# Optimization experiments

Measured on AMD Instinct MI355X. Metric: run time of the kernel, lower is better.

Reference implementation:

```python
import jax, jax.numpy as jnp
import numpy as np

C = 1.0          # curvature of PoincareBall
SQRT_C = 1.0
MIN_NORM = 1e-15
PROJ_EPS = 4e-3  # float32 boundary eps used by PoincareBall.proj
N_NODES = 50000


def _norm(x):
    return jnp.clip(jnp.linalg.norm(x, axis=-1, keepdims=True), MIN_NORM)


def _artanh(x):
    return jnp.arctanh(jnp.clip(x, -1.0 + 1e-7, 1.0 - 1e-7))


def proj(x):
    # clip points to the open ball of radius (1-eps)/sqrt(c)
    norm = _norm(x)
    maxnorm = (1.0 - PROJ_EPS) / SQRT_C
    return jnp.where(norm > maxnorm, x / norm * maxnorm, x)


def expmap0(u):
    u_norm = _norm(u)
    return jnp.tanh(SQRT_C * u_norm) * u / (SQRT_C * u_norm)


def logmap0(p):
    p_norm = _norm(p)
    return _artanh(SQRT_C * p_norm) * p / (SQRT_C * p_norm)


def mobius_add(x, y):
    x2 = jnp.sum(x * x, -1, keepdims=True)
    y2 = jnp.sum(y * y, -1, keepdims=True)
    xy = jnp.sum(x * y, -1, keepdims=True)
    num = (1.0 + 2.0 * C * xy + C * y2) * x + (1.0 - C * x2) * y
    den = 1.0 + 2.0 * C * xy + C * C * x2 * y2
    return num / jnp.clip(den, MIN_NORM)


def mobius_matvec(m, x):
    x_norm = _norm(x)
    mx = x @ m.T  # [N, d_out]
    mx_norm = _norm(mx)
    res = jnp.tanh(mx_norm / x_norm * _artanh(SQRT_C * x_norm)) * mx / (mx_norm * SQRT_C)
    zero_row = jnp.all(mx == 0, axis=-1, keepdims=True)
    return jnp.where(zero_row, jnp.zeros_like(res), res)


def setup_inputs() -> dict:
    key = jax.random.key(0)
    k = jax.random.split(key, 6)
    n, d_in, d_out, n_edges = N_NODES, 256, 96, 800000
    # points on the Poincare ball
    x = proj(0.02 * jax.random.normal(k[0], (n, d_in), jnp.float32))
    weight = jax.random.normal(k[1], (d_out, d_in), jnp.float32) * (1.0 / np.sqrt(d_in)).astype(np.float32)
    bias = jax.random.normal(k[2], (d_out,), jnp.float32) * 0.01
    edge_row = jax.random.randint(k[3], (n_edges,), 0, n)
    edge_col = jax.random.randint(k[4], (n_edges,), 0, n)
    # normalized adjacency weights ~ 1/avg_degree
    edge_weight = jax.random.uniform(k[5], (n_edges,), jnp.float32) * (1.0 / 16.0)
    return {"x": x, "weight": weight, "bias": bias, "edge_weight": edge_weight,
            "edge_row": edge_row, "edge_col": edge_col}


def reference(x, weight, bias, edge_weight, edge_row, edge_col):
    # --- HypLinear (dropout inactive in eval) ---
    h = proj(mobius_matvec(weight, x))
    hyp_bias = proj(expmap0(bias[None, :]))  # proj_tan0 is identity on the ball
    h = proj(mobius_add(h, hyp_bias))
    # --- HypAgg: spmm(adj, logmap0(h)) then expmap0 ---
    xt = logmap0(h)                                  # [N, d_out]
    msgs = edge_weight[:, None] * xt[edge_col]       # [E, d_out]
    support = jax.ops.segment_sum(msgs, edge_row, num_segments=N_NODES)
    h = proj(expmap0(support))
    # --- HypAct: relu in tangent space, map back (c_in == c_out) ---
    h = proj(expmap0(jax.nn.relu(logmap0(h))))
    return h
```

## Files before the change

kernel.cpp:

```cpp
#include <hip/hip_runtime.h>


typedef __attribute__((ext_vector_type(8))) short short8;
typedef __attribute__((ext_vector_type(4))) float floatx4;

#define DIN 256
#define DOUT 96
#define MAXN 0.996f
#define EPS15 1e-15f
#define ATC (1.0f - 1e-7f)
#define NBK 391
#define CAP 3072
#define TILE 3072

__device__ __forceinline__ float us2f(unsigned short u) {
    unsigned int v = ((unsigned int)u) << 16;
    return __uint_as_float(v);
}
__device__ __forceinline__ unsigned short f2us(float f) {
    unsigned int b = __float_as_uint(f);
    unsigned int r = (b + 0x7FFFu + ((b >> 16) & 1u)) >> 16;
    return (unsigned short)r;
}

__global__ void initzero_kernel(const unsigned short* __restrict__ xraw,
                                const void* __restrict__ bias,
                                const void* __restrict__ wgt,
                                float* __restrict__ ws,
                                int* __restrict__ gcur) {
    int i = blockIdx.x * blockDim.x + threadIdx.x;
    int stride = gridDim.x * blockDim.x;
    for (int k = i; k < NBK * 16; k += stride) gcur[k] = 0;

    if (blockIdx.x == 0 && threadIdx.x < 64) {
        int l = threadIdx.x;
        float v0 = us2f(xraw[l]);
        float v1 = us2f(xraw[64 + l]);
        int big = (!(fabsf(v0) < 1e4f)) || (!(fabsf(v1) < 1e4f));
        #pragma unroll
        for (int m = 32; m >= 1; m >>= 1) big |= __shfl_xor(big, m, 64);
        bool isb = !big;
        if (l == 0) ws[97] = isb ? 1.0f : 0.0f;

        float b0 = isb ? us2f(((const unsigned short*)bias)[l])
                       : ((const float*)bias)[l];
        float b1 = 0.0f;
        if (l < 32)
            b1 = isb ? us2f(((const unsigned short*)bias)[64 + l])
                     : ((const float*)bias)[64 + l];
        float n2 = b0 * b0 + b1 * b1;
        #pragma unroll
        for (int m = 32; m >= 1; m >>= 1) n2 += __shfl_xor(n2, m, 64);
        float bn = fmaxf(sqrtf(n2), EPS15);
        float ef = tanhf(bn) / bn;
        float hn = ef * sqrtf(n2);
        float s = (hn > MAXN) ? MAXN / fmaxf(hn, EPS15) : 1.0f;
        ws[l] = s * ef * b0;
        if (l < 32) ws[64 + l] = s * ef * b1;
        if (l == 0) { float v = s * hn; ws[96] = v * v; }
    }

    if (blockIdx.x >= 1 && blockIdx.x <= 12) {
        int t = threadIdx.x, lane = t & 63;
        float v0 = us2f(xraw[lane]);
        float v1 = us2f(xraw[64 + lane]);
        int big = (!(fabsf(v0) < 1e4f)) || (!(fabsf(v1) < 1e4f));
        #pragma unroll
        for (int m = 32; m >= 1; m >>= 1) big |= __shfl_xor(big, m, 64);
        bool isb = !big;
        uint4* wz = (uint4*)(ws + 128);
        int g = t + 256 * (int)(blockIdx.x - 1);
        int c = g >> 5, j = g & 31;
        int f = c >> 4, mr = c & 15;
        int kt = j >> 2, q = j & 3;
        if (isb) {
            const uint4* wg = (const uint4*)wgt;
            wz[(f * 8 + kt) * 64 + q * 16 + mr] = wg[g];
        } else {
            const float* wgf = (const float*)wgt;
            const float* src = wgf + (size_t)c * DIN + j * 8;
            unsigned short tmp[8];
            #pragma unroll
            for (int z = 0; z < 8; z++) tmp[z] = f2us(src[z]);
            wz[(f * 8 + kt) * 64 + q * 16 + mr] = *(const uint4*)tmp;
        }
    }
}

__global__ void __launch_bounds__(256) part_kernel(
        const void* __restrict__ ew,
        const int* __restrict__ erow,
        const int* __restrict__ ecol,
        const float* __restrict__ ws,
        int* __restrict__ gcur,
        uint2* __restrict__ arena, int E) {
    __shared__ uint2 stage[TILE];
    __shared__ int h[NBK], excl[NBK], cur[NBK], gb[NBK];
    __shared__ int cb[64];

    const int t = threadIdx.x;
    const bool isb = ws[97] != 0.0f;
    const int tb = blockIdx.x * TILE;
    const int tcnt = min(TILE, E - tb);

    for (int i = t; i < NBK; i += 256) h[i] = 0;
    __syncthreads();

    int rw[12]; unsigned int pk[12];
    #pragma unroll
    for (int k = 0; k < 12; k++) {
        int e = tb + t + 256 * k;
        if (e < E) {
            int r = erow[e];
            unsigned int wb = isb ? (unsigned int)((const unsigned short*)ew)[e]
                                  : (unsigned int)f2us(((const float*)ew)[e]);
            rw[k] = r;
            pk[k] = (wb << 16) | (unsigned int)ecol[e];
            atomicAdd(&h[r >> 7], 1);
        } else rw[k] = -1;
    }
    __syncthreads();

    if (t < 64) {
        int s = 0;
        #pragma unroll
        for (int j = 0; j < 8; j++) {
            int b2 = t * 8 + j;
            if (b2 < NBK) s += h[b2];
        }
        int sc = s;
        #pragma unroll
        for (int d = 1; d < 64; d <<= 1) {
            int tt = __shfl_up(sc, d, 64);
            if (t >= d) sc += tt;
        }
        cb[t] = sc - s;
    }
    __syncthreads();
    for (int b2 = t; b2 < NBK; b2 += 256) {
        int base = cb[b2 >> 3];
        int x = 0;
        for (int j = (b2 & ~7); j < b2; j++) x += h[j];
        excl[b2] = base + x;
        cur[b2]  = base + x;
        gb[b2] = atomicAdd(&gcur[b2 * 16], h[b2]);
    }
    __syncthreads();

    #pragma unroll
    for (int k = 0; k < 12; k++) {
        if (rw[k] >= 0) {
            int b2 = rw[k] >> 7;
            int slot = atomicAdd(&cur[b2], 1);
            stage[slot] = make_uint2(pk[k], (unsigned int)rw[k]);
        }
    }
    __syncthreads();

    for (int s = t; s < tcnt; s += 256) {
        uint2 ent = stage[s];
        int b2 = (int)ent.y >> 7;
        int p = gb[b2] + (s - excl[b2]);
        if (p < CAP) arena[(size_t)b2 * CAP + p] = ent;
    }
}

__global__ void hyp_kernel(const void* __restrict__ x,
                           float* __restrict__ ws,
                           unsigned short* __restrict__ xtb,
                           int N) {
    const int t = threadIdx.x;
    const bool isb = ws[97] != 0.0f;
    const int lane = t & 63;
    const int wv = t >> 6;
    const int mrow = lane & 15;
    const int quad = lane >> 4;
    const uint4* __restrict__ Wg = (const uint4*)(ws + 128);

    const int r0 = ((int)blockIdx.x * 4 + wv) * 16;
    if (r0 >= N) return;

    float hbl[6];
    #pragma unroll
    for (int f = 0; f < 6; f++) hbl[f] = ws[mrow + 16 * f];
    const float hb2 = ws[96];

    int xr = r0 + mrow; if (xr >= N) xr = N - 1;
    short8 afrag[8];
    if (isb) {
        const unsigned short* xrow = (const unsigned short*)x + (size_t)xr * DIN + quad * 8;
        #pragma unroll
        for (int kt = 0; kt < 8; kt++)
            afrag[kt] = *(const short8*)(xrow + kt * 32);
    } else {
        const float* xrow = (const float*)x + (size_t)xr * DIN + quad * 8;
        #pragma unroll
        for (int kt = 0; kt < 8; kt++) {
            short8 a;
            #pragma unroll
            for (int j = 0; j < 8; j++) a[j] = (short)f2us(xrow[kt * 32 + j]);
            afrag[kt] = a;
        }
    }

    float xn2p = 0.f;
    #pragma unroll
    for (int kt = 0; kt < 8; kt++)
        #pragma unroll
        for (int j = 0; j < 8; j++) {
            float v = us2f((unsigned short)afrag[kt][j]);
            xn2p = fmaf(v, v, xn2p);
        }
    xn2p += __shfl_xor(xn2p, 16, 64);
    xn2p += __shfl_xor(xn2p, 32, 64);

    floatx4 acc[6];
    #pragma unroll
    for (int f = 0; f < 6; f++) acc[f] = (floatx4){0.f, 0.f, 0.f, 0.f};
    #pragma unroll
    for (int f = 0; f < 6; f++) {
        uint4 bw[8];
        #pragma unroll
        for (int kt = 0; kt < 8; kt++)
            bw[kt] = Wg[(f * 8 + kt) * 64 + lane];
        #pragma unroll
        for (int kt = 0; kt < 8; kt++) {
            short8 bfr = *(const short8*)&bw[kt];
            acc[f] = __builtin_amdgcn_mfma_f32_16x16x32_bf16(afrag[kt], bfr, acc[f], 0, 0, 0);
        }
    }

    float mxn2[4], dmh[4];
    #pragma unroll
    for (int reg = 0; reg < 4; reg++) {
        float a2 = 0.f, ad = 0.f;
        #pragma unroll
        for (int f = 0; f < 6; f++) {
            float v = acc[f][reg];
            a2 = fmaf(v, v, a2);
            ad = fmaf(v, hbl[f], ad);
        }
        mxn2[reg] = a2; dmh[reg] = ad;
    }
    #pragma unroll
    for (int m = 8; m >= 1; m >>= 1)
        #pragma unroll
        for (int reg = 0; reg < 4; reg++) {
            mxn2[reg] += __shfl_xor(mxn2[reg], m, 64);
            dmh[reg]  += __shfl_xor(dmh[reg],  m, 64);
        }

    int sel = mrow & 3;
    float xn2  = __shfl(xn2p, quad * 4 + sel, 64);
    float wmx2 = mxn2[sel], wdmh = dmh[sel];

    float xn  = fmaxf(sqrtf(xn2), EPS15);
    float mxn = fmaxf(sqrtf(wmx2), EPS15);
    float g   = (mxn / xn) * atanhf(fminf(xn, ATC));
    float tg  = tanhf(g);
    float rs0 = tg / mxn;
    float rn  = rs0 * sqrtf(wmx2);
    float s1  = (rn > MAXN) ? MAXN / fmaxf(rn, EPS15) : 1.0f;
    float al  = s1 * rs0;
    float x2  = al * al * wmx2;
    float xy  = al * wdmh;
    float cA  = 1.0f + 2.0f * xy + hb2;
    float cB  = 1.0f - x2;
    float den = fmaxf(1.0f + 2.0f * xy + x2 * hb2, EPS15);
    float p   = cA * al / den;
    float qq  = cB / den;
    float o2  = p*p*wmx2 + 2.0f*p*qq*wdmh + qq*qq*hb2;
    float on  = sqrtf(fmaxf(o2, 0.0f));
    float s2  = (on > MAXN) ? MAXN / fmaxf(on, EPS15) : 1.0f;
    float pn  = fmaxf(s2 * on, EPS15);
    float F   = (atanhf(fminf(pn, ATC)) / pn) * s2;
    float Fp_m = F * p, Fq_m = F * qq;

    float Fp[4], Fq[4];
    #pragma unroll
    for (int reg = 0; reg < 4; reg++) {
        Fp[reg] = __shfl(Fp_m, quad * 16 + reg, 64);
        Fq[reg] = __shfl(Fq_m, quad * 16 + reg, 64);
    }

    #pragma unroll
    for (int reg = 0; reg < 4; reg++) {
        int row = r0 + quad * 4 + reg;
        if (row < N) {
            size_t base = (size_t)row * DOUT + mrow;
            #pragma unroll
            for (int f = 0; f < 6; f++)
                xtb[base + 16 * f] = f2us(fmaf(Fp[reg], acc[f][reg], Fq[reg] * hbl[f]));
        }
    }
}

__global__ void __launch_bounds__(256) sortg_kernel(
        const int* __restrict__ gcur,
        uint2* __restrict__ arena,
        uint2* __restrict__ roff) {
    __shared__ int h[128], h8[128], excl[128], cur[128];

    const int t = threadIdx.x;
    const int idx = blockIdx.x;
    int cnt = gcur[idx * 16]; if (cnt > CAP) cnt = CAP;
    const size_t ab = (size_t)idx * CAP;

    for (int i = t; i < 128; i += 256) h[i] = 0;
    __syncthreads();

    uint2 ent[12];
    #pragma unroll
    for (int k = 0; k < 12; k++) {
        int j = t + 256 * k;
        if (j < cnt) {
            ent[k] = arena[ab + j];
            atomicAdd(&h[ent[k].y & 127u], 1);
        } else ent[k] = make_uint2(0u, 0u);
    }
    __syncthreads();

    if (t < 64) {
        int a0 = h[2 * t], a1 = h[2 * t + 1];
        int p0 = (a0 + 7) & ~7, p1 = (a1 + 7) & ~7;
        int ps = p0 + p1;
        int sc = ps;
        #pragma unroll
        for (int d = 1; d < 64; d <<= 1) {
            int tt = __shfl_up(sc, d, 64);
            if (t >= d) sc += tt;
        }
        int ex = sc - ps;
        h8[2 * t] = p0;        h8[2 * t + 1] = p1;
        excl[2 * t] = ex;      excl[2 * t + 1] = ex + p0;
        cur[2 * t]  = ex;      cur[2 * t + 1]  = ex + p0;
    }
    __syncthreads();

    if (t < 128) {
        int e8 = excl[t];
        int c8 = h8[t];
        if (e8 > CAP) e8 = CAP;
        if (e8 + c8 > CAP) c8 = CAP - e8;
        if (c8 < 0) c8 = 0;
        roff[idx * 128 + t] =
            make_uint2((unsigned int)(ab + e8), (unsigned int)c8);
        for (int j = excl[t] + h[t]; j < excl[t] + h8[t]; j++)
            if (j < CAP) arena[ab + j] = make_uint2(0u, 0u);
    }
    #pragma unroll
    for (int k = 0; k < 12; k++) {
        int j = t + 256 * k;
        if (j < cnt) {
            int slot = atomicAdd(&cur[ent[k].y & 127u], 1);
            if (slot < CAP)
                arena[ab + slot] =
                    make_uint2((ent[k].x & 0xFFFFu) * 192u,
                               ent[k].x & 0xFFFF0000u);
        }
    }
}

__global__ void __launch_bounds__(256) rowagg_kernel(
        const unsigned short* __restrict__ xtb,
        const uint2* __restrict__ arena,
        const uint2* __restrict__ roff,
        const float* __restrict__ ws,
        void* __restrict__ out, int N) {
    int wv = threadIdx.x >> 6, lane = threadIdx.x & 63;
    int node = blockIdx.x * 4 + wv;
    if (node >= N) return;
    const bool isb = ws[97] != 0.0f;
    const bool act = lane < 48;

    uint2 ro = roff[node];
    unsigned int start = ro.x;
    int cnt8 = (int)ro.y;

    const char* __restrict__ xc = (const char*)xtb;
    const unsigned int lane4 = (unsigned int)lane * 4u;

    float acc0 = 0.f, acc1 = 0.f;
    unsigned int uA[8], uB[8];
    float wA[8], wB[8];

#define ISSUE(BU, BW, B)                                                       \
    _Pragma("unroll")                                                          \
    for (int k = 0; k < 8; k++) {                                              \
        int idx = (B) * 8 + k;                                                 \
        unsigned int off = (unsigned int)__shfl((int)my.x, idx, 64);           \
        BW[k] = __uint_as_float((unsigned int)__shfl((int)my.y, idx, 64));     \
        BU[k] = *(const unsigned int*)(xc + off + lane4);                      \
    }

#define CONSUME(BU, BW)                                                        \
    _Pragma("unroll")                                                          \
    for (int k = 0; k < 8; k++) {                                              \
        acc0 = fmaf(BW[k], __uint_as_float(BU[k] << 16), acc0);                \
        acc1 = fmaf(BW[k], __uint_as_float(BU[k] & 0xFFFF0000u), acc1);        \
    }

    for (int cs = 0; cs < cnt8; cs += 64) {
        int navail = cnt8 - cs; if (navail > 64) navail = 64;
        uint2 my = arena[start + cs + lane];
        int nb = navail >> 3;
        ISSUE(uA, wA, 0);
        for (int bb = 1; bb < nb; bb++) {
            if (bb & 1) { ISSUE(uB, wB, bb); CONSUME(uA, wA); }
            else        { ISSUE(uA, wA, bb); CONSUME(uB, wB); }
        }
        if (nb & 1) { CONSUME(uA, wA); }
        else        { CONSUME(uB, wB); }
    }
#undef ISSUE
#undef CONSUME

    if (!act) { acc0 = 0.f; acc1 = 0.f; }

    float u0 = acc0, u1 = acc1;
    float n2 = u0*u0 + u1*u1;
    #pragma unroll
    for (int m = 32; m >= 1; m >>= 1) n2 += __shfl_xor(n2, m, 64);
    float un = fmaxf(sqrtf(n2), EPS15);
    float ef = tanhf(un) / un;
    float p0 = ef * u0, p1 = ef * u1;
    float pnrm = ef * sqrtf(n2);
    float sc = (pnrm > MAXN) ? MAXN / fmaxf(pnrm, EPS15) : 1.0f;
    p0 *= sc; p1 *= sc; pnrm *= sc;
    float pncl = fmaxf(pnrm, EPS15);
    float lf = atanhf(fminf(pncl, ATC)) / pncl;
    float t0 = fmaxf(lf * p0, 0.0f), t1 = fmaxf(lf * p1, 0.0f);
    float tn2 = t0*t0 + t1*t1;
    #pragma unroll
    for (int m = 32; m >= 1; m >>= 1) tn2 += __shfl_xor(tn2, m, 64);
    float tn = fmaxf(sqrtf(tn2), EPS15);
    float ef2 = tanhf(tn) / tn;
    float en = ef2 * sqrtf(tn2);
    float s2 = (en > MAXN) ? MAXN / fmaxf(en, EPS15) : 1.0f;
    float scale = s2 * ef2;
    float v0 = scale * t0, v1 = scale * t1;

    if (act) {
        if (isb) {
            unsigned int pk = ((unsigned int)f2us(v1) << 16) | (unsigned int)f2us(v0);
            ((unsigned int*)((unsigned short*)out + (size_t)node * DOUT))[lane] = pk;
        } else {
            float2 fv; fv.x = v0; fv.y = v1;
            ((float2*)((float*)out + (size_t)node * DOUT))[lane] = fv;
        }
    }
}

extern "C" void kernel_launch(void* const* d_in, const int* in_sizes, int n_in,
                              void* d_out, int out_size, void* d_ws, size_t ws_size,
                              hipStream_t stream) {
    const void* x    = d_in[0];
    const void* wgt  = d_in[1];
    const void* bias = d_in[2];
    const void* ew   = d_in[3];
    const int* erow  = (const int*)d_in[4];
    const int* ecol  = (const int*)d_in[5];

    int N = out_size / DOUT;
    int E = in_sizes[4];

    float* wsf = (float*)d_ws;
    int* gcur = (int*)(wsf + 128 + 12288);
    uint2* arena = (uint2*)((char*)d_ws + 74688);
    unsigned short* xtb = (unsigned short*)((char*)d_ws + 74688 + (size_t)NBK * CAP * 8);
    uint2* roff = (uint2*)(xtb + (size_t)N * DOUT);

    int Pb = (E + TILE - 1) / TILE;
    int Hb = (N + 63) / 64;

    initzero_kernel<<<13, 256, 0, stream>>>((const unsigned short*)x, bias, wgt, wsf, gcur);
    part_kernel<<<Pb, 256, 0, stream>>>(ew, erow, ecol, wsf, gcur, arena, E);
    hyp_kernel<<<Hb, 256, 0, stream>>>(x, wsf, xtb, N);
    sortg_kernel<<<NBK, 256, 0, stream>>>(gcur, arena, roff);
    rowagg_kernel<<<(N + 3) / 4, 256, 0, stream>>>(xtb, arena, roff, wsf, d_out, N);
}
```

Before: 184.2 us.

## Fuse pipeline stages into one persistent cooperative kernel with grid syncs

Merges the five separate launches (init, partition, hyperbolic linear, bucket sort, row aggregation) into a single persistent cooperative mega-kernel. Stages are separated by grid-wide barriers, and each stage's work is spread over a grid capped at 1024 blocks, with hyp work and bucket sorting sharing one phase. The partition tile shrinks to fit the shared-memory budget for four blocks per CU. The aim is to remove per-launch overhead and inter-kernel gaps. In exchange it adds grid-sync costs and gives the grid-stride loops less parallelism than the original per-kernel grids, with a multi-launch fallback if cooperative launch fails.

```diff
diff --git a/kernel.cpp b/kernel.cpp
--- a/kernel.cpp
+++ b/kernel.cpp
@@ -1,4 +1,7 @@
 #include <hip/hip_runtime.h>
+#include <hip/hip_cooperative_groups.h>
+
+namespace cg = cooperative_groups;
 
 
 typedef __attribute__((ext_vector_type(8))) short short8;
@@ -11,7 +14,7 @@
 #define ATC (1.0f - 1e-7f)
 #define NBK 391
 #define CAP 3072
-#define TILE 3072
+#define TILE 1024
 
 __device__ __forceinline__ float us2f(unsigned short u) {
     unsigned int v = ((unsigned int)u) << 16;
@@ -23,25 +26,13 @@
     return (unsigned short)r;
 }
 
-__global__ void initzero_kernel(const unsigned short* __restrict__ xraw,
-                                const void* __restrict__ bias,
-                                const void* __restrict__ wgt,
-                                float* __restrict__ ws,
-                                int* __restrict__ gcur) {
-    int i = blockIdx.x * blockDim.x + threadIdx.x;
-    int stride = gridDim.x * blockDim.x;
-    for (int k = i; k < NBK * 16; k += stride) gcur[k] = 0;
-
-    if (blockIdx.x == 0 && threadIdx.x < 64) {
-        int l = threadIdx.x;
-        float v0 = us2f(xraw[l]);
-        float v1 = us2f(xraw[64 + l]);
-        int big = (!(fabsf(v0) < 1e4f)) || (!(fabsf(v1) < 1e4f));
-        #pragma unroll
-        for (int m = 32; m >= 1; m >>= 1) big |= __shfl_xor(big, m, 64);
-        bool isb = !big;
-        if (l == 0) ws[97] = isb ? 1.0f : 0.0f;
-
+__device__ void phase0(const void* bias, const void* wgt,
+                       float* ws, int* gcur, bool isb,
+                       int bid, int t, int G) {
+    for (int k = bid * 256 + t; k < NBK * 16; k += G * 256) gcur[k] = 0;
+
+    if (bid == 0 && t < 64) {
+        int l = t;
         float b0 = isb ? us2f(((const unsigned short*)bias)[l])
                        : ((const float*)bias)[l];
         float b1 = 0.0f;
@@ -59,17 +50,9 @@
         if (l < 32) ws[64 + l] = s * ef * b1;
         if (l == 0) { float v = s * hn; ws[96] = v * v; }
     }
-
-    if (blockIdx.x >= 1 && blockIdx.x <= 12) {
-        int t = threadIdx.x, lane = t & 63;
-        float v0 = us2f(xraw[lane]);
-        float v1 = us2f(xraw[64 + lane]);
-        int big = (!(fabsf(v0) < 1e4f)) || (!(fabsf(v1) < 1e4f));
-        #pragma unroll
-        for (int m = 32; m >= 1; m >>= 1) big |= __shfl_xor(big, m, 64);
-        bool isb = !big;
+    if (bid >= 1 && bid <= 12) {
         uint4* wz = (uint4*)(ws + 128);
-        int g = t + 256 * (int)(blockIdx.x - 1);
+        int g = t + 256 * (bid - 1);
         int c = g >> 5, j = g & 31;
         int f = c >> 4, mr = c & 15;
         int kt = j >> 2, q = j & 3;
@@ -87,302 +70,290 @@
     }
 }
 
-__global__ void __launch_bounds__(256) part_kernel(
-        const void* __restrict__ ew,
-        const int* __restrict__ erow,
-        const int* __restrict__ ecol,
-        const float* __restrict__ ws,
-        int* __restrict__ gcur,
-        uint2* __restrict__ arena, int E) {
-    __shared__ uint2 stage[TILE];
-    __shared__ int h[NBK], excl[NBK], cur[NBK], gb[NBK];
-    __shared__ int cb[64];
-
-    const int t = threadIdx.x;
-    const bool isb = ws[97] != 0.0f;
-    const int tb = blockIdx.x * TILE;
-    const int tcnt = min(TILE, E - tb);
-
-    for (int i = t; i < NBK; i += 256) h[i] = 0;
-    __syncthreads();
-
-    int rw[12]; unsigned int pk[12];
-    #pragma unroll
-    for (int k = 0; k < 12; k++) {
-        int e = tb + t + 256 * k;
-        if (e < E) {
-            int r = erow[e];
-            unsigned int wb = isb ? (unsigned int)((const unsigned short*)ew)[e]
-                                  : (unsigned int)f2us(((const float*)ew)[e]);
-            rw[k] = r;
-            pk[k] = (wb << 16) | (unsigned int)ecol[e];
-            atomicAdd(&h[r >> 7], 1);
-        } else rw[k] = -1;
-    }
-    __syncthreads();
-
-    if (t < 64) {
-        int s = 0;
+__device__ void phase1(const void* ew, const int* erow, const int* ecol,
+                       int* gcur, uint2* arena, int E, bool isb,
+                       int bid, int t, int G,
+                       uint2* stage, int* sh_h, int* sh_e, int* sh_c,
+                       int* sh_g, int* cb) {
+    for (int tile = bid; tile * TILE < E; tile += G) {
+        const int tb = tile * TILE;
+        const int tcnt = min(TILE, E - tb);
+
+        for (int i = t; i < NBK; i += 256) sh_h[i] = 0;
+        __syncthreads();
+
+        int rw[4]; unsigned int pk[4];
         #pragma unroll
-        for (int j = 0; j < 8; j++) {
-            int b2 = t * 8 + j;
-            if (b2 < NBK) s += h[b2];
-        }
-        int sc = s;
+        for (int k = 0; k < 4; k++) {
+            int e = tb + t + 256 * k;
+            if (e < E) {
+                int r = erow[e];
+                unsigned int wb = isb ? (unsigned int)((const unsigned short*)ew)[e]
+                                      : (unsigned int)f2us(((const float*)ew)[e]);
+                rw[k] = r;
+                pk[k] = (wb << 16) | (unsigned int)ecol[e];
+                atomicAdd(&sh_h[r >> 7], 1);
+            } else rw[k] = -1;
+        }
+        __syncthreads();
+
+        if (t < 64) {
+            int s = 0;
+            #pragma unroll
+            for (int j = 0; j < 8; j++) {
+                int b2 = t * 8 + j;
+                if (b2 < NBK) s += sh_h[b2];
+            }
+            int sc = s;
+            #pragma unroll
+            for (int d = 1; d < 64; d <<= 1) {
+                int tt = __shfl_up(sc, d, 64);
+                if (t >= d) sc += tt;
+            }
+            cb[t] = sc - s;
+        }
+        __syncthreads();
+        for (int b2 = t; b2 < NBK; b2 += 256) {
+            int base = cb[b2 >> 3];
+            int xx = 0;
+            for (int j = (b2 & ~7); j < b2; j++) xx += sh_h[j];
+            sh_e[b2] = base + xx;
+            sh_c[b2] = base + xx;
+            sh_g[b2] = atomicAdd(&gcur[b2 * 16], sh_h[b2]);
+        }
+        __syncthreads();
+
         #pragma unroll
-        for (int d = 1; d < 64; d <<= 1) {
-            int tt = __shfl_up(sc, d, 64);
-            if (t >= d) sc += tt;
-        }
-        cb[t] = sc - s;
-    }
-    __syncthreads();
-    for (int b2 = t; b2 < NBK; b2 += 256) {
-        int base = cb[b2 >> 3];
-        int x = 0;
-        for (int j = (b2 & ~7); j < b2; j++) x += h[j];
-        excl[b2] = base + x;
-        cur[b2]  = base + x;
-        gb[b2] = atomicAdd(&gcur[b2 * 16], h[b2]);
-    }
-    __syncthreads();
-
-    #pragma unroll
-    for (int k = 0; k < 12; k++) {
-        if (rw[k] >= 0) {
-            int b2 = rw[k] >> 7;
-            int slot = atomicAdd(&cur[b2], 1);
-            stage[slot] = make_uint2(pk[k], (unsigned int)rw[k]);
-        }
-    }
-    __syncthreads();
-
-    for (int s = t; s < tcnt; s += 256) {
-        uint2 ent = stage[s];
-        int b2 = (int)ent.y >> 7;
-        int p = gb[b2] + (s - excl[b2]);
-        if (p < CAP) arena[(size_t)b2 * CAP + p] = ent;
-    }
-}
-
-__global__ void hyp_kernel(const void* __restrict__ x,
-                           float* __restrict__ ws,
-                           unsigned short* __restrict__ xtb,
-                           int N) {
-    const int t = threadIdx.x;
-    const bool isb = ws[97] != 0.0f;
+        for (int k = 0; k < 4; k++) {
+            if (rw[k] >= 0) {
+                int b2 = rw[k] >> 7;
+                int slot = atomicAdd(&sh_c[b2], 1);
+                stage[slot] = make_uint2(pk[k], (unsigned int)rw[k]);
+            }
+        }
+        __syncthreads();
+
+        for (int s = t; s < tcnt; s += 256) {
+            uint2 ent = stage[s];
+            int b2 = (int)ent.y >> 7;
+            int p = sh_g[b2] + (s - sh_e[b2]);
+            if (p < CAP) arena[(size_t)b2 * CAP + p] = ent;
+        }
+        __syncthreads();
+    }
+}
+
+__device__ void phase2(const void* x, float* ws, unsigned short* xtb,
+                       const int* gcur, uint2* arena, uint2* roff,
+                       int N, bool isb, int bid, int t, int G,
+                       int* sh_h, int* sh_e, int* sh_c, int* sh_g) {
     const int lane = t & 63;
     const int wv = t >> 6;
-    const int mrow = lane & 15;
-    const int quad = lane >> 4;
-    const uint4* __restrict__ Wg = (const uint4*)(ws + 128);
-
-    const int r0 = ((int)blockIdx.x * 4 + wv) * 16;
-    if (r0 >= N) return;
-
-    float hbl[6];
-    #pragma unroll
-    for (int f = 0; f < 6; f++) hbl[f] = ws[mrow + 16 * f];
-    const float hb2 = ws[96];
-
-    int xr = r0 + mrow; if (xr >= N) xr = N - 1;
-    short8 afrag[8];
-    if (isb) {
-        const unsigned short* xrow = (const unsigned short*)x + (size_t)xr * DIN + quad * 8;
-        #pragma unroll
-        for (int kt = 0; kt < 8; kt++)
-            afrag[kt] = *(const short8*)(xrow + kt * 32);
-    } else {
-        const float* xrow = (const float*)x + (size_t)xr * DIN + quad * 8;
-        #pragma unroll
-        for (int kt = 0; kt < 8; kt++) {
-            short8 a;
-            #pragma unroll
-            for (int j = 0; j < 8; j++) a[j] = (short)f2us(xrow[kt * 32 + j]);
-            afrag[kt] = a;
-        }
-    }
-
-    float xn2p = 0.f;
-    #pragma unroll
-    for (int kt = 0; kt < 8; kt++)
-        #pragma unroll
-        for (int j = 0; j < 8; j++) {
-            float v = us2f((unsigned short)afrag[kt][j]);
-            xn2p = fmaf(v, v, xn2p);
-        }
-    xn2p += __shfl_xor(xn2p, 16, 64);
-    xn2p += __shfl_xor(xn2p, 32, 64);
-
-    floatx4 acc[6];
-    #pragma unroll
-    for (int f = 0; f < 6; f++) acc[f] = (floatx4){0.f, 0.f, 0.f, 0.f};
-    #pragma unroll
-    for (int f = 0; f < 6; f++) {
-        uint4 bw[8];
-        #pragma unroll
-        for (int kt = 0; kt < 8; kt++)
-            bw[kt] = Wg[(f * 8 + kt) * 64 + lane];
-        #pragma unroll
-        for (int kt = 0; kt < 8; kt++) {
-            short8 bfr = *(const short8*)&bw[kt];
-            acc[f] = __builtin_amdgcn_mfma_f32_16x16x32_bf16(afrag[kt], bfr, acc[f], 0, 0, 0);
-        }
-    }
-
-    float mxn2[4], dmh[4];
-    #pragma unroll
-    for (int reg = 0; reg < 4; reg++) {
-        float a2 = 0.f, ad = 0.f;
-        #pragma unroll
-        for (int f = 0; f < 6; f++) {
-            float v = acc[f][reg];
-            a2 = fmaf(v, v, a2);
-            ad = fmaf(v, hbl[f], ad);
-        }
-        mxn2[reg] = a2; dmh[reg] = ad;
-    }
-    #pragma unroll
-    for (int m = 8; m >= 1; m >>= 1)
-        #pragma unroll
-        for (int reg = 0; reg < 4; reg++) {
-            mxn2[reg] += __shfl_xor(mxn2[reg], m, 64);
-            dmh[reg]  += __shfl_xor(dmh[reg],  m, 64);
-        }
-
-    int sel = mrow & 3;
-    float xn2  = __shfl(xn2p, quad * 4 + sel, 64);
-    float wmx2 = mxn2[sel], wdmh = dmh[sel];
-
-    float xn  = fmaxf(sqrtf(xn2), EPS15);
-    float mxn = fmaxf(sqrtf(wmx2), EPS15);
-    float g   = (mxn / xn) * atanhf(fminf(xn, ATC));
-    float tg  = tanhf(g);
-    float rs0 = tg / mxn;
-    float rn  = rs0 * sqrtf(wmx2);
-    float s1  = (rn > MAXN) ? MAXN / fmaxf(rn, EPS15) : 1.0f;
-    float al  = s1 * rs0;
-    float x2  = al * al * wmx2;
-    float xy  = al * wdmh;
-    float cA  = 1.0f + 2.0f * xy + hb2;
-    float cB  = 1.0f - x2;
-    float den = fmaxf(1.0f + 2.0f * xy + x2 * hb2, EPS15);
-    float p   = cA * al / den;
-    float qq  = cB / den;
-    float o2  = p*p*wmx2 + 2.0f*p*qq*wdmh + qq*qq*hb2;
-    float on  = sqrtf(fmaxf(o2, 0.0f));
-    float s2  = (on > MAXN) ? MAXN / fmaxf(on, EPS15) : 1.0f;
-    float pn  = fmaxf(s2 * on, EPS15);
-    float F   = (atanhf(fminf(pn, ATC)) / pn) * s2;
-    float Fp_m = F * p, Fq_m = F * qq;
-
-    float Fp[4], Fq[4];
-    #pragma unroll
-    for (int reg = 0; reg < 4; reg++) {
-        Fp[reg] = __shfl(Fp_m, quad * 16 + reg, 64);
-        Fq[reg] = __shfl(Fq_m, quad * 16 + reg, 64);
-    }
-
-    #pragma unroll
-    for (int reg = 0; reg < 4; reg++) {
-        int row = r0 + quad * 4 + reg;
-        if (row < N) {
-            size_t base = (size_t)row * DOUT + mrow;
-            #pragma unroll
-            for (int f = 0; f < 6; f++)
-                xtb[base + 16 * f] = f2us(fmaf(Fp[reg], acc[f][reg], Fq[reg] * hbl[f]));
-        }
-    }
-}
-
-__global__ void __launch_bounds__(256) sortg_kernel(
-        const int* __restrict__ gcur,
-        uint2* __restrict__ arena,
-        uint2* __restrict__ roff) {
-    __shared__ int h[128], h8[128], excl[128], cur[128];
-
-    const int t = threadIdx.x;
-    const int idx = blockIdx.x;
-    int cnt = gcur[idx * 16]; if (cnt > CAP) cnt = CAP;
-    const size_t ab = (size_t)idx * CAP;
-
-    for (int i = t; i < 128; i += 256) h[i] = 0;
-    __syncthreads();
-
-    uint2 ent[12];
-    #pragma unroll
-    for (int k = 0; k < 12; k++) {
-        int j = t + 256 * k;
-        if (j < cnt) {
-            ent[k] = arena[ab + j];
-            atomicAdd(&h[ent[k].y & 127u], 1);
-        } else ent[k] = make_uint2(0u, 0u);
-    }
-    __syncthreads();
-
-    if (t < 64) {
-        int a0 = h[2 * t], a1 = h[2 * t + 1];
-        int p0 = (a0 + 7) & ~7, p1 = (a1 + 7) & ~7;
-        int ps = p0 + p1;
-        int sc = ps;
-        #pragma unroll
-        for (int d = 1; d < 64; d <<= 1) {
-            int tt = __shfl_up(sc, d, 64);
-            if (t >= d) sc += tt;
-        }
-        int ex = sc - ps;
-        h8[2 * t] = p0;        h8[2 * t + 1] = p1;
-        excl[2 * t] = ex;      excl[2 * t + 1] = ex + p0;
-        cur[2 * t]  = ex;      cur[2 * t + 1]  = ex + p0;
-    }
-    __syncthreads();
-
-    if (t < 128) {
-        int e8 = excl[t];
-        int c8 = h8[t];
-        if (e8 > CAP) e8 = CAP;
-        if (e8 + c8 > CAP) c8 = CAP - e8;
-        if (c8 < 0) c8 = 0;
-        roff[idx * 128 + t] =
-            make_uint2((unsigned int)(ab + e8), (unsigned int)c8);
-        for (int j = excl[t] + h[t]; j < excl[t] + h8[t]; j++)
-            if (j < CAP) arena[ab + j] = make_uint2(0u, 0u);
-    }
-    #pragma unroll
-    for (int k = 0; k < 12; k++) {
-        int j = t + 256 * k;
-        if (j < cnt) {
-            int slot = atomicAdd(&cur[ent[k].y & 127u], 1);
-            if (slot < CAP)
-                arena[ab + slot] =
-                    make_uint2((ent[k].x & 0xFFFFu) * 192u,
-                               ent[k].x & 0xFFFF0000u);
-        }
-    }
-}
-
-__global__ void __launch_bounds__(256) rowagg_kernel(
-        const unsigned short* __restrict__ xtb,
-        const uint2* __restrict__ arena,
-        const uint2* __restrict__ roff,
-        const float* __restrict__ ws,
-        void* __restrict__ out, int N) {
-    int wv = threadIdx.x >> 6, lane = threadIdx.x & 63;
-    int node = blockIdx.x * 4 + wv;
-    if (node >= N) return;
-    const bool isb = ws[97] != 0.0f;
+    const int hypu = (N + 63) >> 6;
+    for (int u = bid; u < hypu + NBK; u += G) {
+        if (u < hypu) {
+            const int mrow = lane & 15;
+            const int quad = lane >> 4;
+            const uint4* __restrict__ Wg = (const uint4*)(ws + 128);
+            const int r0 = (u * 4 + wv) * 16;
+            if (r0 < N) {
+                float hbl[6];
+                #pragma unroll
+                for (int f = 0; f < 6; f++) hbl[f] = ws[mrow + 16 * f];
+                const float hb2 = ws[96];
+
+                int xr = r0 + mrow; if (xr >= N) xr = N - 1;
+                short8 afrag[8];
+                if (isb) {
+                    const unsigned short* xrow = (const unsigned short*)x + (size_t)xr * DIN + quad * 8;
+                    #pragma unroll
+                    for (int kt = 0; kt < 8; kt++)
+                        afrag[kt] = *(const short8*)(xrow + kt * 32);
+                } else {
+                    const float* xrow = (const float*)x + (size_t)xr * DIN + quad * 8;
+                    #pragma unroll
+                    for (int kt = 0; kt < 8; kt++) {
+                        short8 a;
+                        #pragma unroll
+                        for (int j = 0; j < 8; j++) a[j] = (short)f2us(xrow[kt * 32 + j]);
+                        afrag[kt] = a;
+                    }
+                }
+
+                float xn2p = 0.f;
+                #pragma unroll
+                for (int kt = 0; kt < 8; kt++)
+                    #pragma unroll
+                    for (int j = 0; j < 8; j++) {
+                        float v = us2f((unsigned short)afrag[kt][j]);
+                        xn2p = fmaf(v, v, xn2p);
+                    }
+                xn2p += __shfl_xor(xn2p, 16, 64);
+                xn2p += __shfl_xor(xn2p, 32, 64);
+
+                floatx4 acc[6];
+                #pragma unroll
+                for (int f = 0; f < 6; f++) acc[f] = (floatx4){0.f, 0.f, 0.f, 0.f};
+                #pragma unroll
+                for (int f = 0; f < 6; f++) {
+                    uint4 bw[8];
+                    #pragma unroll
+                    for (int kt = 0; kt < 8; kt++)
+                        bw[kt] = Wg[(f * 8 + kt) * 64 + lane];
+                    #pragma unroll
+                    for (int kt = 0; kt < 8; kt++) {
+                        short8 bfr = *(const short8*)&bw[kt];
+                        acc[f] = __builtin_amdgcn_mfma_f32_16x16x32_bf16(afrag[kt], bfr, acc[f], 0, 0, 0);
+                    }
+                }
+
+                float mxn2[4], dmh[4];
+                #pragma unroll
+                for (int reg = 0; reg < 4; reg++) {
+                    float a2 = 0.f, ad = 0.f;
+                    #pragma unroll
+                    for (int f = 0; f < 6; f++) {
+                        float v = acc[f][reg];
+                        a2 = fmaf(v, v, a2);
+                        ad = fmaf(v, hbl[f], ad);
+                    }
+                    mxn2[reg] = a2; dmh[reg] = ad;
+                }
+                #pragma unroll
+                for (int m = 8; m >= 1; m >>= 1)
+                    #pragma unroll
+                    for (int reg = 0; reg < 4; reg++) {
+                        mxn2[reg] += __shfl_xor(mxn2[reg], m, 64);
+                        dmh[reg]  += __shfl_xor(dmh[reg],  m, 64);
+                    }
+
+                int sel = mrow & 3;
+                float xn2  = __shfl(xn2p, quad * 4 + sel, 64);
+                float wmx2 = mxn2[sel], wdmh = dmh[sel];
+
+                float xn  = fmaxf(sqrtf(xn2), EPS15);
+                float mxn = fmaxf(sqrtf(wmx2), EPS15);
+                float g   = (mxn / xn) * atanhf(fminf(xn, ATC));
+                float tg  = tanhf(g);
+                float rs0 = tg / mxn;
+                float rn  = rs0 * sqrtf(wmx2);
+                float s1  = (rn > MAXN) ? MAXN / fmaxf(rn, EPS15) : 1.0f;
+                float al  = s1 * rs0;
+                float x2  = al * al * wmx2;
+                float xy  = al * wdmh;
+                float cA  = 1.0f + 2.0f * xy + hb2;
+                float cB  = 1.0f - x2;
+                float den = fmaxf(1.0f + 2.0f * xy + x2 * hb2, EPS15);
+                float p   = cA * al / den;
+                float qq  = cB / den;
+                float o2  = p*p*wmx2 + 2.0f*p*qq*wdmh + qq*qq*hb2;
+                float on  = sqrtf(fmaxf(o2, 0.0f));
+                float s2  = (on > MAXN) ? MAXN / fmaxf(on, EPS15) : 1.0f;
+                float pn  = fmaxf(s2 * on, EPS15);
+                float F   = (atanhf(fminf(pn, ATC)) / pn) * s2;
+                float Fp_m = F * p, Fq_m = F * qq;
+
+                float Fp[4], Fq[4];
+                #pragma unroll
+                for (int reg = 0; reg < 4; reg++) {
+                    Fp[reg] = __shfl(Fp_m, quad * 16 + reg, 64);
+                    Fq[reg] = __shfl(Fq_m, quad * 16 + reg, 64);
+                }
+
+                #pragma unroll
+                for (int reg = 0; reg < 4; reg++) {
+                    int row = r0 + quad * 4 + reg;
+                    if (row < N) {
+                        size_t base = (size_t)row * DOUT + mrow;
+                        #pragma unroll
+                        for (int f = 0; f < 6; f++)
+                            xtb[base + 16 * f] = f2us(fmaf(Fp[reg], acc[f][reg], Fq[reg] * hbl[f]));
+                    }
+                }
+            }
+        } else {
+            const int idx = u - hypu;
+            int cnt = gcur[idx * 16]; if (cnt > CAP) cnt = CAP;
+            const size_t ab = (size_t)idx * CAP;
+
+            for (int i = t; i < 128; i += 256) sh_h[i] = 0;
+            __syncthreads();
+
+            uint2 ent[12];
+            #pragma unroll
+            for (int k = 0; k < 12; k++) {
+                int j = t + 256 * k;
+                if (j < cnt) {
+                    ent[k] = arena[ab + j];
+                    atomicAdd(&sh_h[ent[k].y & 127u], 1);
+                } else ent[k] = make_uint2(0u, 0u);
+            }
+            __syncthreads();
+
+            if (t < 64) {
+                int a0 = sh_h[2 * t], a1 = sh_h[2 * t + 1];
+                int p0 = (a0 + 7) & ~7, p1 = (a1 + 7) & ~7;
+                int ps = p0 + p1;
+                int sc = ps;
+                #pragma unroll
+                for (int d = 1; d < 64; d <<= 1) {
+                    int tt = __shfl_up(sc, d, 64);
+                    if (t >= d) sc += tt;
+                }
+                int ex = sc - ps;
+                sh_g[2 * t] = p0;      sh_g[2 * t + 1] = p1;
+                sh_e[2 * t] = ex;      sh_e[2 * t + 1] = ex + p0;
+                sh_c[2 * t] = ex;      sh_c[2 * t + 1] = ex + p0;
+            }
+            __syncthreads();
+
+            if (t < 128) {
+                int e8 = sh_e[t];
+                int c8 = sh_g[t];
+                if (e8 > CAP) e8 = CAP;
+                if (e8 + c8 > CAP) c8 = CAP - e8;
+                if (c8 < 0) c8 = 0;
+                roff[idx * 128 + t] =
+                    make_uint2((unsigned int)(ab + e8), (unsigned int)c8);
+                for (int j = sh_e[t] + sh_h[t]; j < sh_e[t] + sh_g[t]; j++)
+                    if (j < CAP) arena[ab + j] = make_uint2(0u, 0u);
+            }
+            #pragma unroll
+            for (int k = 0; k < 12; k++) {
+                int j = t + 256 * k;
+                if (j < cnt) {
+                    int slot = atomicAdd(&sh_c[ent[k].y & 127u], 1);
+                    if (slot < CAP)
+                        arena[ab + slot] =
+                            make_uint2((ent[k].x & 0xFFFFu) * 192u,
+                                       ent[k].x & 0xFFFF0000u);
+                }
+            }
+            __syncthreads();
+        }
+    }
+}
+
+__device__ void phase3(const unsigned short* xtb, const uint2* arena,
+                       const uint2* roff, void* out, int N, bool isb,
+                       int bid, int t, int G) {
+    const int lane = t & 63;
+    const int wv = t >> 6;
     const bool act = lane < 48;
-
-    uint2 ro = roff[node];
-    unsigned int start = ro.x;
-    int cnt8 = (int)ro.y;
-
     const char* __restrict__ xc = (const char*)xtb;
     const unsigned int lane4 = (unsigned int)lane * 4u;
-
-    float acc0 = 0.f, acc1 = 0.f;
-    unsigned int uA[8], uB[8];
-    float wA[8], wB[8];
+    const int q4 = (N + 3) >> 2;
+
+    for (int q = bid; q < q4; q += G) {
+        int node = q * 4 + wv;
+        if (node < N) {
+            uint2 ro = roff[node];
+            unsigned int start = ro.x;
+            int cnt8 = (int)ro.y;
+
+            float acc0 = 0.f, acc1 = 0.f;
+            unsigned int uA[8], uB[8];
+            float wA[8], wB[8];
 
 #define ISSUE(BU, BW, B)                                                       \
     _Pragma("unroll")                                                          \
@@ -400,82 +371,168 @@
         acc1 = fmaf(BW[k], __uint_as_float(BU[k] & 0xFFFF0000u), acc1);        \
     }
 
-    for (int cs = 0; cs < cnt8; cs += 64) {
-        int navail = cnt8 - cs; if (navail > 64) navail = 64;
-        uint2 my = arena[start + cs + lane];
-        int nb = navail >> 3;
-        ISSUE(uA, wA, 0);
-        for (int bb = 1; bb < nb; bb++) {
-            if (bb & 1) { ISSUE(uB, wB, bb); CONSUME(uA, wA); }
-            else        { ISSUE(uA, wA, bb); CONSUME(uB, wB); }
-        }
-        if (nb & 1) { CONSUME(uA, wA); }
-        else        { CONSUME(uB, wB); }
-    }
+            for (int cs = 0; cs < cnt8; cs += 64) {
+                int navail = cnt8 - cs; if (navail > 64) navail = 64;
+                uint2 my = arena[start + cs + lane];
+                int nb = navail >> 3;
+                ISSUE(uA, wA, 0);
+                for (int bb = 1; bb < nb; bb++) {
+                    if (bb & 1) { ISSUE(uB, wB, bb); CONSUME(uA, wA); }
+                    else        { ISSUE(uA, wA, bb); CONSUME(uB, wB); }
+                }
+                if (nb & 1) { CONSUME(uA, wA); }
+                else        { CONSUME(uB, wB); }
+            }
 #undef ISSUE
 #undef CONSUME
 
-    if (!act) { acc0 = 0.f; acc1 = 0.f; }
-
-    float u0 = acc0, u1 = acc1;
-    float n2 = u0*u0 + u1*u1;
-    #pragma unroll
-    for (int m = 32; m >= 1; m >>= 1) n2 += __shfl_xor(n2, m, 64);
-    float un = fmaxf(sqrtf(n2), EPS15);
-    float ef = tanhf(un) / un;
-    float p0 = ef * u0, p1 = ef * u1;
-    float pnrm = ef * sqrtf(n2);
-    float sc = (pnrm > MAXN) ? MAXN / fmaxf(pnrm, EPS15) : 1.0f;
-    p0 *= sc; p1 *= sc; pnrm *= sc;
-    float pncl = fmaxf(pnrm, EPS15);
-    float lf = atanhf(fminf(pncl, ATC)) / pncl;
-    float t0 = fmaxf(lf * p0, 0.0f), t1 = fmaxf(lf * p1, 0.0f);
-    float tn2 = t0*t0 + t1*t1;
-    #pragma unroll
-    for (int m = 32; m >= 1; m >>= 1) tn2 += __shfl_xor(tn2, m, 64);
-    float tn = fmaxf(sqrtf(tn2), EPS15);
-    float ef2 = tanhf(tn) / tn;
-    float en = ef2 * sqrtf(tn2);
-    float s2 = (en > MAXN) ? MAXN / fmaxf(en, EPS15) : 1.0f;
-    float scale = s2 * ef2;
-    float v0 = scale * t0, v1 = scale * t1;
-
-    if (act) {
-        if (isb) {
-            unsigned int pk = ((unsigned int)f2us(v1) << 16) | (unsigned int)f2us(v0);
-            ((unsigned int*)((unsigned short*)out + (size_t)node * DOUT))[lane] = pk;
-        } else {
-            float2 fv; fv.x = v0; fv.y = v1;
-            ((float2*)((float*)out + (size_t)node * DOUT))[lane] = fv;
-        }
+            if (!act) { acc0 = 0.f; acc1 = 0.f; }
+
+            float u0 = acc0, u1 = acc1;
+            float n2 = u0*u0 + u1*u1;
+            #pragma unroll
+            for (int m = 32; m >= 1; m >>= 1) n2 += __shfl_xor(n2, m, 64);
+            float un = fmaxf(sqrtf(n2), EPS15);
+            float ef = tanhf(un) / un;
+            float p0 = ef * u0, p1 = ef * u1;
+            float pnrm = ef * sqrtf(n2);
+            float sc = (pnrm > MAXN) ? MAXN / fmaxf(pnrm, EPS15) : 1.0f;
+            p0 *= sc; p1 *= sc; pnrm *= sc;
+            float pncl = fmaxf(pnrm, EPS15);
+            float lf = atanhf(fminf(pncl, ATC)) / pncl;
+            float t0 = fmaxf(lf * p0, 0.0f), t1 = fmaxf(lf * p1, 0.0f);
+            float tn2 = t0*t0 + t1*t1;
+            #pragma unroll
+            for (int m = 32; m >= 1; m >>= 1) tn2 += __shfl_xor(tn2, m, 64);
+            float tn = fmaxf(sqrtf(tn2), EPS15);
+            float ef2 = tanhf(tn) / tn;
+            float en = ef2 * sqrtf(tn2);
+            float s2 = (en > MAXN) ? MAXN / fmaxf(en, EPS15) : 1.0f;
+            float scale = s2 * ef2;
+            float v0 = scale * t0, v1 = scale * t1;
+
+            if (act) {
+                if (isb) {
+                    unsigned int pk = ((unsigned int)f2us(v1) << 16) | (unsigned int)f2us(v0);
+                    ((unsigned int*)((unsigned short*)out + (size_t)node * DOUT))[lane] = pk;
+                } else {
+                    float2 fv; fv.x = v0; fv.y = v1;
+                    ((float2*)((float*)out + (size_t)node * DOUT))[lane] = fv;
+                }
+            }
+        }
+    }
+}
+
+__global__ void __launch_bounds__(256, 4) mega_kernel(
+        const void* __restrict__ x,
+        const void* __restrict__ wgt,
+        const void* __restrict__ bias,
+        const void* __restrict__ ew,
+        const int* __restrict__ erow,
+        const int* __restrict__ ecol,
+        float* __restrict__ ws,
+        void* __restrict__ out,
+        int N, int E, int mode) {
+    __shared__ uint2 stage[TILE];
+    __shared__ int sh_h[NBK], sh_e[NBK], sh_c[NBK], sh_g[NBK];
+    __shared__ int cb[64];
+
+    const int t = threadIdx.x;
+    const int bid = blockIdx.x;
+    const int G = gridDim.x;
+    const int lane = t & 63;
+
+    int* gcur = (int*)(ws + 128 + 12288);
+    uint2* arena = (uint2*)((char*)(void*)ws + 74688);
+    unsigned short* xtb = (unsigned short*)((char*)(void*)ws + 74688 + (size_t)NBK * CAP * 8);
+    uint2* roff = (uint2*)(xtb + (size_t)N * DOUT);
+
+    const unsigned short* xraw = (const unsigned short*)x;
+    bool isb;
+    {
+        float v0 = us2f(xraw[lane]);
+        float v1 = us2f(xraw[64 + lane]);
+        int big = (!(fabsf(v0) < 1e4f)) || (!(fabsf(v1) < 1e4f));
+        #pragma unroll
+        for (int m = 32; m >= 1; m >>= 1) big |= __shfl_xor(big, m, 64);
+        isb = !big;
+    }
+
+    if (mode < 0) {
+        cg::grid_group grid = cg::this_grid();
+        phase0(bias, wgt, ws, gcur, isb, bid, t, G);
+        __threadfence(); grid.sync(); __threadfence();
+        phase1(ew, erow, ecol, gcur, arena, E, isb, bid, t, G,
+               stage, sh_h, sh_e, sh_c, sh_g, cb);
+        __threadfence(); grid.sync(); __threadfence();
+        phase2(x, ws, xtb, gcur, arena, roff, N, isb, bid, t, G,
+               sh_h, sh_e, sh_c, sh_g);
+        __threadfence(); grid.sync(); __threadfence();
+        phase3(xtb, arena, roff, out, N, isb, bid, t, G);
+    } else if (mode == 0) {
+        phase0(bias, wgt, ws, gcur, isb, bid, t, G);
+    } else if (mode == 1) {
+        phase1(ew, erow, ecol, gcur, arena, E, isb, bid, t, G,
+               stage, sh_h, sh_e, sh_c, sh_g, cb);
+    } else if (mode == 2) {
+        phase2(x, ws, xtb, gcur, arena, roff, N, isb, bid, t, G,
+               sh_h, sh_e, sh_c, sh_g);
+    } else {
+        phase3(xtb, arena, roff, out, N, isb, bid, t, G);
     }
 }
 
 extern "C" void kernel_launch(void* const* d_in, const int* in_sizes, int n_in,
                               void* d_out, int out_size, void* d_ws, size_t ws_size,
                               hipStream_t stream) {
-    const void* x    = d_in[0];
-    const void* wgt  = d_in[1];
-    const void* bias = d_in[2];
-    const void* ew   = d_in[3];
-    const int* erow  = (const int*)d_in[4];
-    const int* ecol  = (const int*)d_in[5];
+    void* x    = d_in[0];
+    void* wgt  = d_in[1];
+    void* bias = d_in[2];
+    void* ew   = d_in[3];
+    void* erow = d_in[4];
+    void* ecol = d_in[5];
 
     int N = out_size / DOUT;
     int E = in_sizes[4];
-
     float* wsf = (float*)d_ws;
-    int* gcur = (int*)(wsf + 128 + 12288);
-    uint2* arena = (uint2*)((char*)d_ws + 74688);
-    unsigned short* xtb = (unsigned short*)((char*)d_ws + 74688 + (size_t)NBK * CAP * 8);
-    uint2* roff = (uint2*)(xtb + (size_t)N * DOUT);
-
-    int Pb = (E + TILE - 1) / TILE;
-    int Hb = (N + 63) / 64;
-
-    initzero_kernel<<<13, 256, 0, stream>>>((const unsigned short*)x, bias, wgt, wsf, gcur);
-    part_kernel<<<Pb, 256, 0, stream>>>(ew, erow, ecol, wsf, gcur, arena, E);
-    hyp_kernel<<<Hb, 256, 0, stream>>>(x, wsf, xtb, N);
-    sortg_kernel<<<NBK, 256, 0, stream>>>(gcur, arena, roff);
-    rowagg_kernel<<<(N + 3) / 4, 256, 0, stream>>>(xtb, arena, roff, wsf, d_out, N);
-}
+    void* outp = d_out;
+
+    static int coop_state = -2;
+    static int coop_grid = 0;
+    if (coop_state == -2) {
+        int nb = 0, ncu = 0;
+        hipError_t e1 = hipOccupancyMaxActiveBlocksPerMultiprocessor(
+            &nb, mega_kernel, 256, 0);
+        hipError_t e2 = hipDeviceGetAttribute(
+            &ncu, hipDeviceAttributeMultiprocessorCount, 0);
+        if (e1 == hipSuccess && e2 == hipSuccess && nb > 0 && ncu > 0) {
+            long g = (long)nb * (long)ncu;
+            coop_grid = (int)(g > 1024 ? 1024 : g);
+            coop_state = (coop_grid >= 64) ? 1 : 0;
+        } else {
+            coop_state = 0;
+        }
+        (void)hipGetLastError();
+    }
+
+    if (coop_state == 1) {
+        int mode = -1;
+        void* kargs[] = {&x, &wgt, &bias, &ew, &erow, &ecol, &wsf, &outp,
+                         &N, &E, &mode};
+        hipError_t err = hipLaunchCooperativeKernel(
+            (void*)mega_kernel, dim3(coop_grid), dim3(256), kargs, 0, stream);
+        if (err == hipSuccess) return;
+        coop_state = 0;
+        (void)hipGetLastError();
+    }
+
+    mega_kernel<<<64, 256, 0, stream>>>(x, wgt, bias, ew, (const int*)erow,
+                                        (const int*)ecol, wsf, outp, N, E, 0);
+    mega_kernel<<<(E + TILE - 1) / TILE, 256, 0, stream>>>(
+        x, wgt, bias, ew, (const int*)erow, (const int*)ecol, wsf, outp, N, E, 1);
+    mega_kernel<<<(N + 63) / 64 + NBK, 256, 0, stream>>>(
+        x, wgt, bias, ew, (const int*)erow, (const int*)ecol, wsf, outp, N, E, 2);
+    mega_kernel<<<(N + 3) / 4, 256, 0, stream>>>(
+        x, wgt, bias, ew, (const int*)erow, (const int*)ecol, wsf, outp, N, E, 3);
+}
```

Result: slower. 718.8 us (+290.2%).

## Merge edge partition and hyperbolic linear kernels into one interleaved launch

Applied to the files above, without the earlier changes.

Fuses the edge-partitioning kernel and the HypLinear/logmap kernel into a single launch whose blocks alternate between partition and matmul roles. Both phases then run concurrently on the GPU and one launch gap goes away. Separately, rowagg now uses 512-thread blocks (8 nodes each), and inactive lanes (48 and above) load from a fixed address instead of a per-lane offset. The risks are the larger shared-memory footprint of the merged kernel, which applies to every block, and the non-uniform work per block.

```diff
diff --git a/kernel.cpp b/kernel.cpp
--- a/kernel.cpp
+++ b/kernel.cpp
@@ -87,97 +87,102 @@
     }
 }
 
-__global__ void __launch_bounds__(256) part_kernel(
+__global__ void __launch_bounds__(256) parthyp_kernel(
+        const void* __restrict__ x,
         const void* __restrict__ ew,
         const int* __restrict__ erow,
         const int* __restrict__ ecol,
-        const float* __restrict__ ws,
+        float* __restrict__ ws,
         int* __restrict__ gcur,
-        uint2* __restrict__ arena, int E) {
+        uint2* __restrict__ arena,
+        unsigned short* __restrict__ xtb,
+        int N, int E, int Pb) {
     __shared__ uint2 stage[TILE];
-    __shared__ int h[NBK], excl[NBK], cur[NBK], gb[NBK];
+    __shared__ int sh_h[NBK], sh_e[NBK], sh_c[NBK], sh_g[NBK];
     __shared__ int cb[64];
 
     const int t = threadIdx.x;
     const bool isb = ws[97] != 0.0f;
-    const int tb = blockIdx.x * TILE;
-    const int tcnt = min(TILE, E - tb);
-
-    for (int i = t; i < NBK; i += 256) h[i] = 0;
-    __syncthreads();
-
-    int rw[12]; unsigned int pk[12];
-    #pragma unroll
-    for (int k = 0; k < 12; k++) {
-        int e = tb + t + 256 * k;
-        if (e < E) {
-            int r = erow[e];
-            unsigned int wb = isb ? (unsigned int)((const unsigned short*)ew)[e]
-                                  : (unsigned int)f2us(((const float*)ew)[e]);
-            rw[k] = r;
-            pk[k] = (wb << 16) | (unsigned int)ecol[e];
-            atomicAdd(&h[r >> 7], 1);
-        } else rw[k] = -1;
-    }
-    __syncthreads();
-
-    if (t < 64) {
-        int s = 0;
-        #pragma unroll
-        for (int j = 0; j < 8; j++) {
-            int b2 = t * 8 + j;
-            if (b2 < NBK) s += h[b2];
-        }
-        int sc = s;
-        #pragma unroll
-        for (int d = 1; d < 64; d <<= 1) {
-            int tt = __shfl_up(sc, d, 64);
-            if (t >= d) sc += tt;
-        }
-        cb[t] = sc - s;
-    }
-    __syncthreads();
-    for (int b2 = t; b2 < NBK; b2 += 256) {
-        int base = cb[b2 >> 3];
-        int x = 0;
-        for (int j = (b2 & ~7); j < b2; j++) x += h[j];
-        excl[b2] = base + x;
-        cur[b2]  = base + x;
-        gb[b2] = atomicAdd(&gcur[b2 * 16], h[b2]);
-    }
-    __syncthreads();
-
-    #pragma unroll
-    for (int k = 0; k < 12; k++) {
-        if (rw[k] >= 0) {
-            int b2 = rw[k] >> 7;
-            int slot = atomicAdd(&cur[b2], 1);
-            stage[slot] = make_uint2(pk[k], (unsigned int)rw[k]);
-        }
-    }
-    __syncthreads();
-
-    for (int s = t; s < tcnt; s += 256) {
-        uint2 ent = stage[s];
-        int b2 = (int)ent.y >> 7;
-        int p = gb[b2] + (s - excl[b2]);
-        if (p < CAP) arena[(size_t)b2 * CAP + p] = ent;
-    }
-}
-
-__global__ void hyp_kernel(const void* __restrict__ x,
-                           float* __restrict__ ws,
-                           unsigned short* __restrict__ xtb,
-                           int N) {
-    const int t = threadIdx.x;
-    const bool isb = ws[97] != 0.0f;
+
+    int b = blockIdx.x;
+    bool ispart; int idx;
+    if (b < 2 * Pb) { ispart = (b & 1); idx = b >> 1; }
+    else            { ispart = false;   idx = b - Pb; }
+
+    if (ispart) {
+        const int tb = idx * TILE;
+        const int tcnt = min(TILE, E - tb);
+
+        for (int i = t; i < NBK; i += 256) sh_h[i] = 0;
+        __syncthreads();
+
+        int rw[12]; unsigned int pk[12];
+        #pragma unroll
+        for (int k = 0; k < 12; k++) {
+            int e = tb + t + 256 * k;
+            if (e < E) {
+                int r = erow[e];
+                unsigned int wb = isb ? (unsigned int)((const unsigned short*)ew)[e]
+                                      : (unsigned int)f2us(((const float*)ew)[e]);
+                rw[k] = r;
+                pk[k] = (wb << 16) | (unsigned int)ecol[e];
+                atomicAdd(&sh_h[r >> 7], 1);
+            } else rw[k] = -1;
+        }
+        __syncthreads();
+
+        if (t < 64) {
+            int s = 0;
+            #pragma unroll
+            for (int j = 0; j < 8; j++) {
+                int b2 = t * 8 + j;
+                if (b2 < NBK) s += sh_h[b2];
+            }
+            int sc = s;
+            #pragma unroll
+            for (int d = 1; d < 64; d <<= 1) {
+                int tt = __shfl_up(sc, d, 64);
+                if (t >= d) sc += tt;
+            }
+            cb[t] = sc - s;
+        }
+        __syncthreads();
+        for (int b2 = t; b2 < NBK; b2 += 256) {
+            int base = cb[b2 >> 3];
+            int xx = 0;
+            for (int j = (b2 & ~7); j < b2; j++) xx += sh_h[j];
+            sh_e[b2] = base + xx;
+            sh_c[b2] = base + xx;
+            sh_g[b2] = atomicAdd(&gcur[b2 * 16], sh_h[b2]);
+        }
+        __syncthreads();
+
+        #pragma unroll
+        for (int k = 0; k < 12; k++) {
+            if (rw[k] >= 0) {
+                int b2 = rw[k] >> 7;
+                int slot = atomicAdd(&sh_c[b2], 1);
+                stage[slot] = make_uint2(pk[k], (unsigned int)rw[k]);
+            }
+        }
+        __syncthreads();
+
+        for (int s = t; s < tcnt; s += 256) {
+            uint2 ent = stage[s];
+            int b2 = (int)ent.y >> 7;
+            int p = sh_g[b2] + (s - sh_e[b2]);
+            if (p < CAP) arena[(size_t)b2 * CAP + p] = ent;
+        }
+        return;
+    }
+
     const int lane = t & 63;
     const int wv = t >> 6;
     const int mrow = lane & 15;
     const int quad = lane >> 4;
     const uint4* __restrict__ Wg = (const uint4*)(ws + 128);
 
-    const int r0 = ((int)blockIdx.x * 4 + wv) * 16;
+    const int r0 = (idx * 4 + wv) * 16;
     if (r0 >= N) return;
 
     float hbl[6];
@@ -361,14 +366,14 @@
     }
 }
 
-__global__ void __launch_bounds__(256) rowagg_kernel(
+__global__ void __launch_bounds__(512) rowagg_kernel(
         const unsigned short* __restrict__ xtb,
         const uint2* __restrict__ arena,
         const uint2* __restrict__ roff,
         const float* __restrict__ ws,
         void* __restrict__ out, int N) {
     int wv = threadIdx.x >> 6, lane = threadIdx.x & 63;
-    int node = blockIdx.x * 4 + wv;
+    int node = blockIdx.x * 8 + wv;
     if (node >= N) return;
     const bool isb = ws[97] != 0.0f;
     const bool act = lane < 48;
@@ -378,7 +383,7 @@
     int cnt8 = (int)ro.y;
 
     const char* __restrict__ xc = (const char*)xtb;
-    const unsigned int lane4 = (unsigned int)lane * 4u;
+    const unsigned int lane4 = act ? (unsigned int)lane * 4u : 0xFFFFFFFFu;
 
     float acc0 = 0.f, acc1 = 0.f;
     unsigned int uA[8], uB[8];
@@ -390,7 +395,8 @@
         int idx = (B) * 8 + k;                                                 \
         unsigned int off = (unsigned int)__shfl((int)my.x, idx, 64);           \
         BW[k] = __uint_as_float((unsigned int)__shfl((int)my.y, idx, 64));     \
-        BU[k] = *(const unsigned int*)(xc + off + lane4);                      \
+        unsigned int a = act ? (off + lane4) : 0u;                             \
+        BU[k] = *(const unsigned int*)(xc + a);                                \
     }
 
 #define CONSUME(BU, BW)                                                        \
@@ -474,8 +480,8 @@
     int Hb = (N + 63) / 64;
 
     initzero_kernel<<<13, 256, 0, stream>>>((const unsigned short*)x, bias, wgt, wsf, gcur);
-    part_kernel<<<Pb, 256, 0, stream>>>(ew, erow, ecol, wsf, gcur, arena, E);
-    hyp_kernel<<<Hb, 256, 0, stream>>>(x, wsf, xtb, N);
+    parthyp_kernel<<<Pb + Hb, 256, 0, stream>>>(x, ew, erow, ecol, wsf, gcur,
+                                                arena, xtb, N, E, Pb);
     sortg_kernel<<<NBK, 256, 0, stream>>>(gcur, arena, roff);
-    rowagg_kernel<<<(N + 3) / 4, 256, 0, stream>>>(xtb, arena, roff, wsf, d_out, N);
-}
+    rowagg_kernel<<<(N + 7) / 8, 512, 0, stream>>>(xtb, arena, roff, wsf, d_out, N);
+}
```

New measurement: 180.3 us. -2.1%, faster.
